# Kernel tuning notes

Measured on AMD Instinct MI355X. Metric: run time of the kernel, lower is better.

The kernel has to match this reference:

```python
import jax, jax.numpy as jnp
import numpy as np

D_MODEL = 1024
NUM_HEADS = 16
D_K = D_MODEL // NUM_HEADS
D_FF = 4096
EPS = 1e-6


def setup_inputs() -> dict:
    key = jax.random.key(0)
    ks = jax.random.split(key, 12)
    B, S = 4, 1024
    s = 1.0 / np.sqrt(D_MODEL)
    return {
        "x": jax.random.normal(ks[0], (B, S, D_MODEL), dtype=jnp.float32),
        "ln1_g": jnp.ones((D_MODEL,), jnp.float32),
        "ln1_b": jnp.zeros((D_MODEL,), jnp.float32),
        "wq": jax.random.normal(ks[1], (D_MODEL, D_MODEL), jnp.float32) * s,
        "wk": jax.random.normal(ks[2], (D_MODEL, D_MODEL), jnp.float32) * s,
        "wv": jax.random.normal(ks[3], (D_MODEL, D_MODEL), jnp.float32) * s,
        "wo": jax.random.normal(ks[4], (D_MODEL, D_MODEL), jnp.float32) * s,
        "ln2_g": jnp.ones((D_MODEL,), jnp.float32),
        "ln2_b": jnp.zeros((D_MODEL,), jnp.float32),
        "w1": jax.random.normal(ks[5], (D_MODEL, D_FF), jnp.float32) * s,
        "b1": jnp.zeros((D_FF,), jnp.float32),
        "w2": jax.random.normal(ks[6], (D_FF, D_MODEL), jnp.float32) * (1.0 / np.sqrt(D_FF)),
        "b2": jnp.zeros((D_MODEL,), jnp.float32),
    }


def _layernorm(x, g, b):
    mu = jnp.mean(x, axis=-1, keepdims=True)
    var = jnp.var(x, axis=-1, keepdims=True)
    return (x - mu) * jax.lax.rsqrt(var + EPS) * g + b


def _mha(x, wq, wk, wv, wo):
    B, S, _ = x.shape
    # project and split heads: [B,S,D] -> [B,H,S,Dk]
    q = (x @ wq).reshape(B, S, NUM_HEADS, D_K).transpose(0, 2, 1, 3)
    k = (x @ wk).reshape(B, S, NUM_HEADS, D_K).transpose(0, 2, 1, 3)
    v = (x @ wv).reshape(B, S, NUM_HEADS, D_K).transpose(0, 2, 1, 3)
    scores = jnp.einsum("bhqd,bhkd->bhqk", q, k) / np.sqrt(D_K).astype(np.float32)
    attn = jax.nn.softmax(scores, axis=-1)  # no mask: source forwards mask=None
    out = jnp.einsum("bhqk,bhkd->bhqd", attn, v)
    out = out.transpose(0, 2, 1, 3).reshape(B, S, D_MODEL)
    return out @ wo


def reference(x, ln1_g, ln1_b, wq, wk, wv, wo, ln2_g, ln2_b, w1, b1, w2, b2):
    x1 = _layernorm(x, ln1_g, ln1_b)
    x = x + _mha(x1, wq, wk, wv, wo)  # dropout identity (eval)
    x2 = _layernorm(x, ln2_g, ln2_b)
    ffn = jax.nn.relu(x2 @ w1 + b1) @ w2 + b2
    return x + ffn
```

## Files before the change

### kernel.cpp

```cpp
#include <hip/hip_runtime.h>

typedef __bf16 bf16;
typedef __bf16 bf16x8 __attribute__((ext_vector_type(8)));
typedef __bf16 bf16x4 __attribute__((ext_vector_type(4)));
typedef float f32x4 __attribute__((ext_vector_type(4)));

__device__ __forceinline__ void gload_lds16(const void* g, void* l) {
  __builtin_amdgcn_global_load_lds(
      (const __attribute__((address_space(1))) unsigned int*)g,
      (__attribute__((address_space(3))) unsigned int*)l, 16, 0, 0);
}

__global__ __launch_bounds__(256) void prep_kernel(
    const float* __restrict__ wq, const float* __restrict__ wk,
    const float* __restrict__ wv, const float* __restrict__ wo,
    bf16* __restrict__ wTqkv, bf16* __restrict__ wTo,
    const float* __restrict__ x, const float* __restrict__ g,
    const float* __restrict__ b, bf16* __restrict__ y) {
  const int id = blockIdx.x;
  if (id < 1024) {
    const int w = threadIdx.x >> 6, lane = threadIdx.x & 63;
    const int row = id * 4 + w;
    const float* xr = x + (size_t)row * 1024;
    float4 v[4];
    float s = 0.f, sq = 0.f;
#pragma unroll
    for (int c = 0; c < 4; c++) {
      v[c] = *reinterpret_cast<const float4*>(xr + c * 256 + lane * 4);
      s += v[c].x + v[c].y + v[c].z + v[c].w;
      sq += v[c].x * v[c].x + v[c].y * v[c].y + v[c].z * v[c].z + v[c].w * v[c].w;
    }
#pragma unroll
    for (int d = 32; d >= 1; d >>= 1) {
      s += __shfl_xor(s, d, 64);
      sq += __shfl_xor(sq, d, 64);
    }
    const float mu = s * (1.f / 1024.f);
    const float rs = rsqrtf(sq * (1.f / 1024.f) - mu * mu + 1e-6f);
#pragma unroll
    for (int c = 0; c < 4; c++) {
      float4 gv = *reinterpret_cast<const float4*>(g + c * 256 + lane * 4);
      float4 bv = *reinterpret_cast<const float4*>(b + c * 256 + lane * 4);
      bf16x4 ov;
      ov[0] = (bf16)((v[c].x - mu) * rs * gv.x + bv.x);
      ov[1] = (bf16)((v[c].y - mu) * rs * gv.y + bv.y);
      ov[2] = (bf16)((v[c].z - mu) * rs * gv.z + bv.z);
      ov[3] = (bf16)((v[c].w - mu) * rs * gv.w + bv.w);
      *reinterpret_cast<bf16x4*>(y + (size_t)row * 1024 + c * 256 + lane * 4) = ov;
    }
    return;
  }
  __shared__ float tile[32][33];
  const int idx = id - 1024;
  const int m = idx >> 10, r = idx & 1023;
  const float* src = m == 0 ? wq : m == 1 ? wk : m == 2 ? wv : wo;
  bf16* dst = m == 3 ? wTo : wTqkv + (size_t)m * 1024 * 1024;
  const int tx = threadIdx.x & 31, ty = threadIdx.x >> 5;
  const int c0 = (r & 31) * 32, r0 = (r >> 5) * 32;
#pragma unroll
  for (int i = 0; i < 4; i++)
    tile[ty + i * 8][tx] = src[(size_t)(r0 + ty + i * 8) * 1024 + c0 + tx];
  __syncthreads();
#pragma unroll
  for (int i = 0; i < 4; i++)
    dst[(size_t)(c0 + ty + i * 8) * 1024 + r0 + tx] = (bf16)tile[tx][ty + i * 8];
}

__global__ __launch_bounds__(256) void reduce_ln_kernel(const bf16* __restrict__ p0,
                                                        const bf16* __restrict__ p1,
                                                        const float* __restrict__ x,
                                                        const float* __restrict__ g,
                                                        const float* __restrict__ b,
                                                        bf16* __restrict__ xres,
                                                        bf16* __restrict__ y) {
  const int w = threadIdx.x >> 6, lane = threadIdx.x & 63;
  const int row = blockIdx.x * 4 + w;
  const size_t rb = (size_t)row * 1024;
  float4 v[4];
  float s = 0.f, sq = 0.f;
#pragma unroll
  for (int c = 0; c < 4; c++) {
    const int off = c * 256 + lane * 4;
    float4 xv = *reinterpret_cast<const float4*>(x + rb + off);
    bf16x4 a0 = *reinterpret_cast<const bf16x4*>(p0 + rb + off);
    bf16x4 a1 = *reinterpret_cast<const bf16x4*>(p1 + rb + off);
    v[c].x = xv.x + (float)a0[0] + (float)a1[0];
    v[c].y = xv.y + (float)a0[1] + (float)a1[1];
    v[c].z = xv.z + (float)a0[2] + (float)a1[2];
    v[c].w = xv.w + (float)a0[3] + (float)a1[3];
    bf16x4 xo;
    xo[0] = (bf16)v[c].x; xo[1] = (bf16)v[c].y;
    xo[2] = (bf16)v[c].z; xo[3] = (bf16)v[c].w;
    *reinterpret_cast<bf16x4*>(xres + rb + off) = xo;
    s += v[c].x + v[c].y + v[c].z + v[c].w;
    sq += v[c].x * v[c].x + v[c].y * v[c].y + v[c].z * v[c].z + v[c].w * v[c].w;
  }
#pragma unroll
  for (int d = 32; d >= 1; d >>= 1) {
    s += __shfl_xor(s, d, 64);
    sq += __shfl_xor(sq, d, 64);
  }
  const float mu = s * (1.f / 1024.f);
  const float rs = rsqrtf(sq * (1.f / 1024.f) - mu * mu + 1e-6f);
#pragma unroll
  for (int c = 0; c < 4; c++) {
    const int off = c * 256 + lane * 4;
    float4 gv = *reinterpret_cast<const float4*>(g + off);
    float4 bv = *reinterpret_cast<const float4*>(b + off);
    bf16x4 ov;
    ov[0] = (bf16)((v[c].x - mu) * rs * gv.x + bv.x);
    ov[1] = (bf16)((v[c].y - mu) * rs * gv.y + bv.y);
    ov[2] = (bf16)((v[c].z - mu) * rs * gv.z + bv.z);
    ov[3] = (bf16)((v[c].w - mu) * rs * gv.w + bv.w);
    *reinterpret_cast<bf16x4*>(y + rb + off) = ov;
  }
}

__global__ __launch_bounds__(256) void reduce_out_kernel(const bf16* __restrict__ p0,
                                                         const bf16* __restrict__ p1,
                                                         const bf16* __restrict__ p2,
                                                         const bf16* __restrict__ p3,
                                                         const float* __restrict__ bias,
                                                         const bf16* __restrict__ xres,
                                                         float* __restrict__ out) {
  const size_t i = ((size_t)blockIdx.x * 256 + threadIdx.x) * 8;
  const int col = (int)(i & 1023);
  bf16x8 a0 = *reinterpret_cast<const bf16x8*>(p0 + i);
  bf16x8 a1 = *reinterpret_cast<const bf16x8*>(p1 + i);
  bf16x8 a2 = *reinterpret_cast<const bf16x8*>(p2 + i);
  bf16x8 a3 = *reinterpret_cast<const bf16x8*>(p3 + i);
  bf16x8 xr = *reinterpret_cast<const bf16x8*>(xres + i);
  float4 b0 = *reinterpret_cast<const float4*>(bias + col);
  float4 b1 = *reinterpret_cast<const float4*>(bias + col + 4);
  float4 o0, o1;
  o0.x = (float)xr[0] + b0.x + (float)a0[0] + (float)a1[0] + (float)a2[0] + (float)a3[0];
  o0.y = (float)xr[1] + b0.y + (float)a0[1] + (float)a1[1] + (float)a2[1] + (float)a3[1];
  o0.z = (float)xr[2] + b0.z + (float)a0[2] + (float)a1[2] + (float)a2[2] + (float)a3[2];
  o0.w = (float)xr[3] + b0.w + (float)a0[3] + (float)a1[3] + (float)a2[3] + (float)a3[3];
  o1.x = (float)xr[4] + b1.x + (float)a0[4] + (float)a1[4] + (float)a2[4] + (float)a3[4];
  o1.y = (float)xr[5] + b1.y + (float)a0[5] + (float)a1[5] + (float)a2[5] + (float)a3[5];
  o1.z = (float)xr[6] + b1.z + (float)a0[6] + (float)a1[6] + (float)a2[6] + (float)a3[6];
  o1.w = (float)xr[7] + b1.w + (float)a0[7] + (float)a1[7] + (float)a2[7] + (float)a3[7];
  *reinterpret_cast<float4*>(out + i) = o0;
  *reinterpret_cast<float4*>(out + i + 4) = o1;
}

template <int EPI>
__global__ __launch_bounds__(256) void gemm_bt(const bf16* __restrict__ A,
                                               const bf16* __restrict__ Bt,
                                               void* __restrict__ Cout,
                                               const float* __restrict__ bias,
                                               int M, int N, int K, int gy, int gxy,
                                               int Kc) {
  __shared__ __align__(16) bf16 As[2][128][32];
  __shared__ __align__(16) bf16 Bs[2][128][32];
  const int tid = threadIdx.x;
  const int w = tid >> 6, lane = tid & 63;
  const int wr = w >> 1, wc = w & 1;

  const int nwg = gridDim.x;
  const int cpx = nwg >> 3;
  const int swz = (blockIdx.x & 7) * cpx + (blockIdx.x >> 3);
  const int chunk = swz / gxy, rem = swz % gxy;
  const int gpc = gy << 3;
  const int band = rem / gpc, r2 = rem % gpc;
  const int bm = (band * 8 + (r2 & 7)) * 128;
  const int bn = (r2 >> 3) * 128;

  f32x4 acc[4][4] = {};
  const int r4 = lane >> 2;
  const int c8 = (lane & 3) * 8;
  const bf16* Ag = A + (size_t)(bm + w * 32 + r4) * K + chunk * Kc + c8;
  const bf16* Bg = Bt + (size_t)(bn + w * 32 + r4) * K + chunk * Kc + c8;
  const int fr = lane & 15, fo = (lane >> 4) * 8;

#define STAGE(buf, k0)                                                 \
  do {                                                                 \
    gload_lds16(Ag + (k0), &As[buf][w * 32][0]);                       \
    gload_lds16(Ag + (size_t)16 * K + (k0), &As[buf][w * 32 + 16][0]); \
    gload_lds16(Bg + (k0), &Bs[buf][w * 32][0]);                       \
    gload_lds16(Bg + (size_t)16 * K + (k0), &Bs[buf][w * 32 + 16][0]); \
  } while (0)

  const int nt = Kc >> 5;
  STAGE(0, 0);
  __syncthreads();
  int cur = 0;
  for (int t = 0; t < nt; ++t) {
    if (t + 1 < nt) STAGE(cur ^ 1, (t + 1) << 5);
    bf16x8 af[4], bfr[4];
#pragma unroll
    for (int m = 0; m < 4; m++)
      af[m] = *reinterpret_cast<const bf16x8*>(&As[cur][wr * 64 + m * 16 + fr][fo]);
#pragma unroll
    for (int n = 0; n < 4; n++)
      bfr[n] = *reinterpret_cast<const bf16x8*>(&Bs[cur][wc * 64 + n * 16 + fr][fo]);
#pragma unroll
    for (int m = 0; m < 4; m++)
#pragma unroll
      for (int n = 0; n < 4; n++)
        acc[m][n] = __builtin_amdgcn_mfma_f32_16x16x32_bf16(af[m], bfr[n], acc[m][n], 0, 0, 0);
    __syncthreads();
    cur ^= 1;
  }
#undef STAGE

  bf16* outp = (bf16*)Cout + (EPI == 3 ? (size_t)chunk * M * N : 0);
  const int cr = (lane >> 4) * 4, cc = lane & 15;
#pragma unroll
  for (int m = 0; m < 4; m++) {
#pragma unroll
    for (int n = 0; n < 4; n++) {
      const int row = bm + wr * 64 + m * 16 + cr;
      const int col = bn + wc * 64 + n * 16 + cc;
#pragma unroll
      for (int r = 0; r < 4; r++) {
        const float va = acc[m][n][r];
        const size_t idx = (size_t)(row + r) * N + col;
        if (EPI == 0 || EPI == 3) {
          outp[idx] = (bf16)va;
        } else {
          const float t = va + bias[col];
          outp[idx] = (bf16)(t > 0.f ? t : 0.f);
        }
      }
    }
  }
}

template <int EPI>
__global__ __launch_bounds__(512, 2) void gemm256(const bf16* __restrict__ A,
                                                  const bf16* __restrict__ Bt,
                                                  void* __restrict__ Cout,
                                                  const float* __restrict__ bias,
                                                  int M, int N, int K, int gy, int gxy,
                                                  int Kc, int ngemm,
                                                  const float* __restrict__ tw1,
                                                  const float* __restrict__ tw2,
                                                  bf16* __restrict__ two1,
                                                  bf16* __restrict__ two2) {
  __shared__ __align__(16) bf16 As[2][256][64];
  __shared__ __align__(16) bf16 Bs[2][256][64];
  const int tid = threadIdx.x;
  const int w = tid >> 6, lane = tid & 63;
  const int wm = w >> 2, wn = w & 3;
  const int fr = lane & 15, g = lane >> 4;

  const int nwg = gridDim.x;
  const int cpx = nwg >> 3;
  const int swz = (blockIdx.x & 7) * cpx + (blockIdx.x >> 3);

  char* AsB = (char*)&As[0][0][0];
  char* BsB = (char*)&Bs[0][0][0];

  if (swz >= ngemm) {
    const int aux = swz - ngemm;
    float* tf = (float*)AsB + (tid >> 8) * (33 * 32);
    const int t8 = tid & 255;
    const int tx = t8 & 31, ty = t8 >> 5;
    const int sub = tid >> 8;

    const float* src; bf16* dst; int R, C, c0, r0;
#define SETJOB(job)                                                     \
    do {                                                                \
      if ((job) < 4096) {                                               \
        src = tw1; dst = two1; R = 1024; C = 4096;                      \
        c0 = ((job) & 127) * 32; r0 = ((job) >> 7) * 32;                \
      } else {                                                          \
        const int j2 = (job) - 4096;                                    \
        src = tw2; dst = two2; R = 4096; C = 1024;                      \
        c0 = (j2 & 31) * 32; r0 = (j2 >> 5) * 32;                       \
      }                                                                 \
    } while (0)

    float cur[4], nxt[4];
    SETJOB(aux * 2 + sub);
#pragma unroll
    for (int i = 0; i < 4; i++)
      cur[i] = src[(size_t)(r0 + ty + i * 8) * C + c0 + tx];
    int pc0 = c0, pr0 = r0, pR = R;
    bf16* pdst = dst;
    for (int t = 0; t < 64; ++t) {
      if (t + 1 < 64) {
        SETJOB((t + 1) * 128 + aux * 2 + sub);
#pragma unroll
        for (int i = 0; i < 4; i++)
          nxt[i] = src[(size_t)(r0 + ty + i * 8) * C + c0 + tx];
      }
#pragma unroll
      for (int i = 0; i < 4; i++) tf[(ty + i * 8) * 33 + tx] = cur[i];
      __syncthreads();
#pragma unroll
      for (int i = 0; i < 4; i++)
        pdst[(size_t)(pc0 + ty + i * 8) * pR + pr0 + tx] = (bf16)tf[tx * 33 + ty + i * 8];
      __syncthreads();
#pragma unroll
      for (int i = 0; i < 4; i++) cur[i] = nxt[i];
      pc0 = c0; pr0 = r0; pR = R; pdst = dst;
    }
#undef SETJOB
    return;
  }

  const int chunk = swz / gxy, rem = swz % gxy;
  const int gpc = gy << 3;
  const int band = rem / gpc, r2 = rem % gpc;
  const int bm = (band * 8 + (r2 & 7)) * 256;
  const int bn = (r2 >> 3) * 256;

  const bf16* Ab = A + (size_t)bm * K;
  const bf16* Bb = Bt + (size_t)bn * K;

  const int lr = lane >> 3;
  const int sle = ((lane & 7) ^ lr) * 8;
  const int rB0 = w * 16;
  const int rB1 = 128 + w * 16;
  const int rA0 = wm * 128 + wn * 16;
  const int rA1 = wm * 128 + 64 + wn * 16;

  const int rowA = (wm * 128 + fr) * 128;
  const int rowB = (wn * 64 + fr) * 128;
  const int colk0 = (g * 16) ^ ((fr & 7) << 4);
  const int colk1 = (64 + g * 16) ^ ((fr & 7) << 4);

  f32x4 acc[8][4] = {};

#define SG8(base, r0, kb, ldsrow)                                           \
  do {                                                                      \
    gload_lds16(base + (size_t)((r0) + lr) * K + (kb) + sle, (ldsrow));     \
    gload_lds16(base + (size_t)((r0) + 8 + lr) * K + (kb) + sle,            \
                (char*)(ldsrow) + 1024);                                    \
  } while (0)

  const int nt = Kc >> 6;
  const int koff = chunk * Kc;

  SG8(Bb, rB0, koff, BsB + rB0 * 128);
  SG8(Bb, rB1, koff, BsB + rB1 * 128);
  SG8(Ab, rA0, koff, AsB + rA0 * 128);
  SG8(Ab, rA1, koff, AsB + rA1 * 128);

#define PHASE_BODY(p, mb)                                                     \
  {                                                                           \
    if ((p) == 0) {                                                           \
      _Pragma("unroll") for (int nf = 0; nf < 4; nf++) {                      \
        bfr[nf][0] = *(const bf16x8*)(Br + rowB + nf * 2048 + colk0);         \
        bfr[nf][1] = *(const bf16x8*)(Br + rowB + nf * 2048 + colk1);         \
      }                                                                       \
    }                                                                         \
    af[0][0] = *(const bf16x8*)(Ar + rowA + (mb)*2048 + colk0);               \
    af[0][1] = *(const bf16x8*)(Ar + rowA + (mb)*2048 + colk1);               \
    af[1][0] = *(const bf16x8*)(Ar + rowA + ((mb) + 1) * 2048 + colk0);       \
    af[1][1] = *(const bf16x8*)(Ar + rowA + ((mb) + 1) * 2048 + colk1);       \
    if (pre) {                                                                \
      if ((p) == 0) SG8(Bb, rB0, kb2, Bw + rB0 * 128);                        \
      if ((p) == 1) SG8(Bb, rB1, kb2, Bw + rB1 * 128);                        \
      if ((p) == 2) SG8(Ab, rA0, kb2, Aw + rA0 * 128);                        \
      if ((p) == 3) SG8(Ab, rA1, kb2, Aw + rA1 * 128);                        \
    }                                                                         \
    __builtin_amdgcn_s_setprio(1);                                            \
    _Pragma("unroll") for (int m2 = 0; m2 < 2; m2++)                          \
        _Pragma("unroll") for (int nf = 0; nf < 4; nf++) {                    \
      acc[(mb) + m2][nf] = __builtin_amdgcn_mfma_f32_16x16x32_bf16(           \
          af[m2][0], bfr[nf][0], acc[(mb) + m2][nf], 0, 0, 0);                \
      acc[(mb) + m2][nf] = __builtin_amdgcn_mfma_f32_16x16x32_bf16(           \
          af[m2][1], bfr[nf][1], acc[(mb) + m2][nf], 0, 0, 0);                \
    }                                                                         \
    __builtin_amdgcn_s_setprio(0);                                            \
  }

  int buf = 0;
  for (int kt = 0; kt < nt; ++kt) {
    char* Ar = AsB + buf * 32768;
    char* Br = BsB + buf * 32768;
    char* Aw = AsB + (buf ^ 1) * 32768;
    char* Bw = BsB + (buf ^ 1) * 32768;
    const bool pre = (kt + 1) < nt;
    const int kb2 = koff + (kt + 1) * 64;
    bf16x8 bfr[4][2];
    bf16x8 af[2][2];

    asm volatile("s_waitcnt vmcnt(2)" ::: "memory");
    __builtin_amdgcn_s_barrier();
    PHASE_BODY(0, 0)

    if (pre) asm volatile("s_waitcnt vmcnt(4)" ::: "memory");
    else     asm volatile("s_waitcnt vmcnt(2)" ::: "memory");
    __builtin_amdgcn_s_barrier();
    PHASE_BODY(1, 2)

    if (pre) asm volatile("s_waitcnt vmcnt(4)" ::: "memory");
    else     asm volatile("s_waitcnt vmcnt(0)" ::: "memory");
    __builtin_amdgcn_s_barrier();
    PHASE_BODY(2, 4)

    if (pre) asm volatile("s_waitcnt vmcnt(6)" ::: "memory");
    else     asm volatile("s_waitcnt vmcnt(0)" ::: "memory");
    __builtin_amdgcn_s_barrier();
    PHASE_BODY(3, 6)

    buf ^= 1;
  }
#undef PHASE_BODY
#undef SG8

  bf16* outp = (bf16*)Cout + (EPI == 3 ? (size_t)chunk * M * N : 0);
  const int cr = g * 4;
#pragma unroll
  for (int mf = 0; mf < 8; mf++) {
#pragma unroll
    for (int nf = 0; nf < 4; nf++) {
      const int row = bm + wm * 128 + mf * 16 + cr;
      const int col = bn + wn * 64 + nf * 16 + fr;
#pragma unroll
      for (int r = 0; r < 4; r++) {
        const float va = acc[mf][nf][r];
        const size_t idx = (size_t)(row + r) * N + col;
        if (EPI == 3 || EPI == 0) {
          outp[idx] = (bf16)va;
        } else {
          const float t = va + bias[col];
          outp[idx] = (bf16)(t > 0.f ? t : 0.f);
        }
      }
    }
  }
}

__global__ __launch_bounds__(512, 4) void attn_kernel(const bf16* __restrict__ Q,
                                                      const bf16* __restrict__ K,
                                                      const bf16* __restrict__ V,
                                                      bf16* __restrict__ O, int ld) {
  __shared__ __align__(16) bf16 Ks[2][64][64];
  __shared__ __align__(16) bf16 Vt[2][64][64];
  __shared__ __align__(16) bf16 Pl[8][16][64];
  const int tid = threadIdx.x;
  const int w = tid >> 6, l = tid & 63;
  const int lo = l & 15, g = l >> 4;
  const int sw = (lo & 7) << 3;

  const int id = blockIdx.x;
  const int bh = id & 63, qb = id >> 6;
  const int b = bh >> 4, h = bh & 15;
  const int hoff = h * 64;
  const size_t rowQ = (size_t)b * 1024 + qb * 128 + w * 16;
  const size_t rowKV0 = (size_t)b * 1024;

  const int srow = tid >> 3, scch = tid & 7;
  const int vcb = w * 8;

  bf16x8 qfr[2];
#pragma unroll
  for (int ds = 0; ds < 2; ds++)
    qfr[ds] = *reinterpret_cast<const bf16x8*>(
        Q + (rowQ + lo) * ld + hoff + ds * 32 + g * 8);

  const float c = 0.18033688f;
  f32x4 lacc = {0.f, 0.f, 0.f, 0.f};
  f32x4 o[4] = {};

  {
    gload_lds16(K + (rowKV0 + srow) * ld + hoff + ((scch ^ (srow & 7)) << 3),
                &Ks[0][w * 8][0]);
    bf16x8 vv = *reinterpret_cast<const bf16x8*>(V + (rowKV0 + l) * ld + hoff + vcb);
#pragma unroll
    for (int j = 0; j < 8; j++) Vt[0][vcb + j][l ^ (j << 3)] = vv[j];
  }
  __syncthreads();

#define ATILE(PAR, KT)                                                               \
  {                                                                                  \
    bf16x8 vv;                                                                       \
    const bool more = (KT) + 1 < 16;                                                 \
    if (more) {                                                                      \
      const size_t rkv = rowKV0 + ((KT) + 1) * 64;                                   \
      gload_lds16(K + (rkv + srow) * ld + hoff + ((scch ^ (srow & 7)) << 3),         \
                  &Ks[(PAR) ^ 1][w * 8][0]);                                         \
      vv = *reinterpret_cast<const bf16x8*>(V + (rkv + l) * ld + hoff + vcb);        \
    }                                                                                \
    f32x4 sa[4] = {};                                                                \
    _Pragma("unroll") for (int ds = 0; ds < 2; ds++) {                               \
      bf16x8 kf[4];                                                                  \
      _Pragma("unroll") for (int kfi = 0; kfi < 4; kfi++)                            \
          kf[kfi] = *reinterpret_cast<const bf16x8*>(                                \
              &Ks[PAR][kfi * 16 + lo][(ds * 32 + g * 8) ^ sw]);                      \
      _Pragma("unroll") for (int kfi = 0; kfi < 4; kfi++)                            \
          sa[kfi] =                                                                  \
              __builtin_amdgcn_mfma_f32_16x16x32_bf16(kf[kfi], qfr[ds], sa[kfi], 0, 0, 0); \
    }                                                                                \
    float p[16];                                                                     \
    _Pragma("unroll") for (int kfi = 0; kfi < 4; kfi++)                              \
        _Pragma("unroll") for (int r = 0; r < 4; r++)                                \
            p[kfi * 4 + r] = exp2f(sa[kfi][r] * c);                                  \
    _Pragma("unroll") for (int r = 0; r < 4; r++)                                    \
        lacc[r] += (p[r] + p[4 + r]) + (p[8 + r] + p[12 + r]);                       \
    _Pragma("unroll") for (int kfi = 0; kfi < 4; kfi++) {                            \
      bf16x4 pk;                                                                     \
      pk[0] = (bf16)p[kfi * 4 + 0];                                                  \
      pk[1] = (bf16)p[kfi * 4 + 1];                                                  \
      pk[2] = (bf16)p[kfi * 4 + 2];                                                  \
      pk[3] = (bf16)p[kfi * 4 + 3];                                                  \
      *reinterpret_cast<bf16x4*>(&Pl[w][lo][(kfi * 16 + g * 4) ^ sw]) = pk;          \
    }                                                                                \
    _Pragma("unroll") for (int ks = 0; ks < 2; ks++) {                               \
      bf16x8 pf = *reinterpret_cast<const bf16x8*>(&Pl[w][lo][(ks * 32 + g * 8) ^ sw]); \
      _Pragma("unroll") for (int df = 0; df < 4; df++) {                             \
        bf16x8 vf = *reinterpret_cast<const bf16x8*>(                                \
            &Vt[PAR][df * 16 + lo][(ks * 32 + g * 8) ^ sw]);                         \
        o[df] = __builtin_amdgcn_mfma_f32_16x16x32_bf16(vf, pf, o[df], 0, 0, 0);     \
      }                                                                              \
    }                                                                                \
    if (more) {                                                                      \
      _Pragma("unroll") for (int j = 0; j < 8; j++)                                  \
          Vt[(PAR) ^ 1][vcb + j][l ^ (j << 3)] = vv[j];                              \
    }                                                                                \
    __syncthreads();                                                                 \
  }

  for (int kt2 = 0; kt2 < 16; kt2 += 2) {
    ATILE(0, kt2)
    ATILE(1, kt2 + 1)
  }
#undef ATILE

  float lsum = (lacc[0] + lacc[1]) + (lacc[2] + lacc[3]);
  lsum += __shfl_xor(lsum, 16);
  lsum += __shfl_xor(lsum, 32);
  const float rl = 1.f / lsum;
#pragma unroll
  for (int df = 0; df < 4; df++) {
    bf16x4 ov;
#pragma unroll
    for (int r = 0; r < 4; r++) ov[r] = (bf16)(o[df][r] * rl);
    *reinterpret_cast<bf16x4*>(&Pl[w][lo][(df * 16 + g * 4) ^ sw]) = ov;
  }
  const int row = l >> 2;
  const int swr = (row & 7) << 3;
  const int c2 = (l & 3) * 16;
#pragma unroll
  for (int i = 0; i < 2; i++) {
    bf16x8 ov = *reinterpret_cast<const bf16x8*>(&Pl[w][row][(c2 + i * 8) ^ swr]);
    *reinterpret_cast<bf16x8*>(O + (rowQ + row) * 1024 + hoff + c2 + i * 8) = ov;
  }
}

extern "C" void kernel_launch(void* const* d_in, const int* in_sizes, int n_in,
                              void* d_out, int out_size, void* d_ws, size_t ws_size,
                              hipStream_t stream) {
  const float* x     = (const float*)d_in[0];
  const float* ln1_g = (const float*)d_in[1];
  const float* ln1_b = (const float*)d_in[2];
  const float* wq    = (const float*)d_in[3];
  const float* wk    = (const float*)d_in[4];
  const float* wv    = (const float*)d_in[5];
  const float* wo    = (const float*)d_in[6];
  const float* ln2_g = (const float*)d_in[7];
  const float* ln2_b = (const float*)d_in[8];
  const float* w1    = (const float*)d_in[9];
  const float* b1    = (const float*)d_in[10];
  const float* w2    = (const float*)d_in[11];
  const float* b2    = (const float*)d_in[12];

  const size_t MB = 1ull << 20;
  char* ws = (char*)d_ws;
  bf16* wTqkv = (bf16*)(ws + 0 * MB);
  bf16* wTo   = (bf16*)(ws + 6 * MB);
  bf16* wT1   = (bf16*)(ws + 8 * MB);
  bf16* wT2   = (bf16*)(ws + 16 * MB);
  bf16* x1    = (bf16*)(ws + 24 * MB);
  bf16* qkv   = (bf16*)(ws + 32 * MB);
  bf16* xres  = (bf16*)(ws + 56 * MB);
  bf16* h1    = (bf16*)(ws + 72 * MB);
  bf16* attn  = x1;
  bf16* x2    = qkv;
  bf16* pOp   = (bf16*)(ws + 40 * MB);
  bf16* pF    = (bf16*)(ws + 24 * MB);

  const dim3 TB(256);

  prep_kernel<<<5120, TB, 0, stream>>>(wq, wk, wv, wo, wTqkv, wTo,
                                       x, ln1_g, ln1_b, x1);

  gemm256<0><<<256, dim3(512), 0, stream>>>(x1, wTqkv, qkv, nullptr,
                                            4096, 3072, 1024, 12, 192, 1024, 192,
                                            w1, w2, wT1, wT2);

  attn_kernel<<<512, dim3(512), 0, stream>>>(qkv, qkv + 1024, qkv + 2048, attn, 3072);

  gemm_bt<3><<<512, TB, 0, stream>>>(attn, wTo, pOp, nullptr, 4096, 1024, 1024, 8, 256, 512);

  reduce_ln_kernel<<<1024, TB, 0, stream>>>(pOp, pOp + 4096 * 1024, x, ln2_g, ln2_b, xres, x2);

  gemm256<2><<<256, dim3(512), 0, stream>>>(x2, wT1, h1, b1,
                                            4096, 4096, 1024, 16, 256, 1024, 256,
                                            nullptr, nullptr, nullptr, nullptr);

  gemm256<3><<<256, dim3(512), 0, stream>>>(h1, wT2, pF, nullptr,
                                            4096, 1024, 4096, 4, 64, 1024, 256,
                                            nullptr, nullptr, nullptr, nullptr);

  reduce_out_kernel<<<2048, TB, 0, stream>>>(pF, pF + 4096 * 1024, pF + 2 * 4096 * 1024,
                                             pF + 3 * 4096 * 1024, b2, xres, (float*)d_out);
}
```

Baseline: 191.5 us.

## Vectorize weight transpose side-work and spread aux blocks evenly across XCDs

The auxiliary blocks inside the QKV GEMM launch, which transpose and convert w1/w2 to bf16, now work on 128x32 tiles. They use 16-byte float4 loads and 16-byte bf16x8 stores instead of scalar accesses. Aux block selection now uses a per-XCD local id, so each XCD runs 24 GEMM tiles and 8 transpose blocks instead of all aux blocks landing on one end of the swizzled order. The aim is more bandwidth-efficient transposes and balanced work per XCD. The trade-off is larger LDS tiles and a fixed dependence on 256 blocks split 32 per XCD.

After: 188.7 us. About the same (-1.5%).

```diff
diff --git a/kernel.cpp b/kernel.cpp
--- a/kernel.cpp
+++ b/kernel.cpp
@@ -234,7 +234,7 @@
                                                   void* __restrict__ Cout,
                                                   const float* __restrict__ bias,
                                                   int M, int N, int K, int gy, int gxy,
-                                                  int Kc, int ngemm,
+                                                  int Kc, int naux,
                                                   const float* __restrict__ tw1,
                                                   const float* __restrict__ tw2,
                                                   bf16* __restrict__ two1,
@@ -253,56 +253,74 @@
   char* AsB = (char*)&As[0][0][0];
   char* BsB = (char*)&Bs[0][0][0];
 
-  if (swz >= ngemm) {
-    const int aux = swz - ngemm;
-    float* tf = (float*)AsB + (tid >> 8) * (33 * 32);
-    const int t8 = tid & 255;
-    const int tx = t8 & 31, ty = t8 >> 5;
-    const int sub = tid >> 8;
-
-    const float* src; bf16* dst; int R, C, c0, r0;
+  int gid = swz;
+  if (naux > 0) {
+    const int lid = swz & 31, xcd = swz >> 5;
+    if (lid >= 24) {
+      const int aux = xcd * 8 + (lid - 24);
+      const int t8 = tid & 255;
+      const int sub = tid >> 8;
+      float* tf = (float*)AsB + sub * (128 * 33);
+      const int lrow = t8 >> 3;
+      const int lcol = (t8 & 7) * 4;
+      const int drow = t8 >> 3;
+      const int dc = (t8 & 7) * 8;
+
+      const float* src; bf16* dst; int R, C, c0, r0;
 #define SETJOB(job)                                                     \
-    do {                                                                \
-      if ((job) < 4096) {                                               \
-        src = tw1; dst = two1; R = 1024; C = 4096;                      \
-        c0 = ((job) & 127) * 32; r0 = ((job) >> 7) * 32;                \
-      } else {                                                          \
-        const int j2 = (job) - 4096;                                    \
-        src = tw2; dst = two2; R = 4096; C = 1024;                      \
-        c0 = (j2 & 31) * 32; r0 = (j2 >> 5) * 32;                       \
-      }                                                                 \
-    } while (0)
-
-    float cur[4], nxt[4];
-    SETJOB(aux * 2 + sub);
-#pragma unroll
-    for (int i = 0; i < 4; i++)
-      cur[i] = src[(size_t)(r0 + ty + i * 8) * C + c0 + tx];
-    int pc0 = c0, pr0 = r0, pR = R;
-    bf16* pdst = dst;
-    for (int t = 0; t < 64; ++t) {
-      if (t + 1 < 64) {
-        SETJOB((t + 1) * 128 + aux * 2 + sub);
-#pragma unroll
-        for (int i = 0; i < 4; i++)
-          nxt[i] = src[(size_t)(r0 + ty + i * 8) * C + c0 + tx];
+      do {                                                              \
+        if ((job) < 1024) {                                             \
+          src = tw1; dst = two1; R = 1024; C = 4096;                    \
+          r0 = ((job) >> 7) * 128; c0 = ((job) & 127) * 32;             \
+        } else {                                                        \
+          const int j2 = (job) - 1024;                                  \
+          src = tw2; dst = two2; R = 4096; C = 1024;                    \
+          r0 = (j2 >> 5) * 128; c0 = (j2 & 31) * 32;                    \
+        }                                                               \
+      } while (0)
+
+      f32x4 cf[4], nf[4];
+      SETJOB(aux * 2 + sub);
+#pragma unroll
+      for (int p = 0; p < 4; p++)
+        cf[p] = *reinterpret_cast<const f32x4*>(
+            &src[(size_t)(r0 + lrow + 32 * p) * C + c0 + lcol]);
+      int c_0 = c0, r_0 = r0, R_0 = R;
+      bf16* d_0 = dst;
+
+      for (int t = 0; t < 16; ++t) {
+        if (t + 1 < 16) {
+          SETJOB((t + 1) * 128 + aux * 2 + sub);
+#pragma unroll
+          for (int p = 0; p < 4; p++)
+            nf[p] = *reinterpret_cast<const f32x4*>(
+                &src[(size_t)(r0 + lrow + 32 * p) * C + c0 + lcol]);
+        }
+#pragma unroll
+        for (int p = 0; p < 4; p++)
+#pragma unroll
+          for (int j = 0; j < 4; j++)
+            tf[(lrow + 32 * p) * 33 + lcol + j] = cf[p][j];
+        __syncthreads();
+        bf16x8 s0, s1;
+#pragma unroll
+        for (int k = 0; k < 8; k++) s0[k] = (bf16)tf[(dc + k) * 33 + drow];
+#pragma unroll
+        for (int k = 0; k < 8; k++) s1[k] = (bf16)tf[(64 + dc + k) * 33 + drow];
+        *reinterpret_cast<bf16x8*>(&d_0[(size_t)(c_0 + drow) * R_0 + r_0 + dc]) = s0;
+        *reinterpret_cast<bf16x8*>(&d_0[(size_t)(c_0 + drow) * R_0 + r_0 + 64 + dc]) = s1;
+        __syncthreads();
+#pragma unroll
+        for (int p = 0; p < 4; p++) cf[p] = nf[p];
+        c_0 = c0; r_0 = r0; R_0 = R; d_0 = dst;
       }
-#pragma unroll
-      for (int i = 0; i < 4; i++) tf[(ty + i * 8) * 33 + tx] = cur[i];
-      __syncthreads();
-#pragma unroll
-      for (int i = 0; i < 4; i++)
-        pdst[(size_t)(pc0 + ty + i * 8) * pR + pr0 + tx] = (bf16)tf[tx * 33 + ty + i * 8];
-      __syncthreads();
-#pragma unroll
-      for (int i = 0; i < 4; i++) cur[i] = nxt[i];
-      pc0 = c0; pr0 = r0; pR = R; pdst = dst;
+#undef SETJOB
+      return;
     }
-#undef SETJOB
-    return;
-  }
-
-  const int chunk = swz / gxy, rem = swz % gxy;
+    gid = xcd * 24 + lid;
+  }
+
+  const int chunk = gid / gxy, rem = gid % gxy;
   const int gpc = gy << 3;
   const int band = rem / gpc, r2 = rem % gpc;
   const int bm = (band * 8 + (r2 & 7)) * 256;
@@ -582,7 +600,7 @@
                                        x, ln1_g, ln1_b, x1);
 
   gemm256<0><<<256, dim3(512), 0, stream>>>(x1, wTqkv, qkv, nullptr,
-                                            4096, 3072, 1024, 12, 192, 1024, 192,
+                                            4096, 3072, 1024, 12, 192, 1024, 64,
                                             w1, w2, wT1, wT2);
 
   attn_kernel<<<512, dim3(512), 0, stream>>>(qkv, qkv + 1024, qkv + 2048, attn, 3072);
@@ -592,11 +610,11 @@
   reduce_ln_kernel<<<1024, TB, 0, stream>>>(pOp, pOp + 4096 * 1024, x, ln2_g, ln2_b, xres, x2);
 
   gemm256<2><<<256, dim3(512), 0, stream>>>(x2, wT1, h1, b1,
-                                            4096, 4096, 1024, 16, 256, 1024, 256,
+                                            4096, 4096, 1024, 16, 256, 1024, 0,
                                             nullptr, nullptr, nullptr, nullptr);
 
   gemm256<3><<<256, dim3(512), 0, stream>>>(h1, wT2, pF, nullptr,
-                                            4096, 1024, 4096, 4, 64, 1024, 256,
+                                            4096, 1024, 4096, 4, 64, 1024, 0,
                                             nullptr, nullptr, nullptr, nullptr);
 
   reduce_out_kernel<<<2048, TB, 0, stream>>>(pF, pF + 4096 * 1024, pF + 2 * 4096 * 1024,
```
